# Kernel optimization log

Hardware: AMD Instinct MI355X
Metric: run time of the kernel (lower is better)

## Reference

```python
import jax, jax.numpy as jnp
import numpy as np

B, L, D = 8, 4096, 128
TEMPERATURE = 1.0


def setup_inputs() -> dict:
    key = jax.random.key(0)
    kx, kw, kb = jax.random.split(key, 3)
    x = jax.random.normal(kx, (B, L, D), dtype=jnp.float32)
    # nn.Linear(dim, dim): weight [D, D], bias [D]
    bound = 1.0 / np.sqrt(D)
    W = jax.random.uniform(kw, (D, D), minval=-bound, maxval=bound, dtype=jnp.float32)
    b = jax.random.uniform(kb, (D,), minval=-bound, maxval=bound, dtype=jnp.float32)
    return {"x": x, "W": W, "b": b}


def reference(x, W, b):
    # projected = proj(x): torch Linear is x @ W.T + b
    projected = jnp.einsum("bld,ed->ble", x, W) + b            # [B, L, D]

    # adaptive_avg_pool1d over sequence length L -> L//2 (L even => pair means)
    Bq, Lx, Dx = x.shape
    q = x.reshape(Bq, Lx // 2, 2, Dx).mean(axis=2)             # [B, L/2, D]
    q = jnp.einsum("bld,ed->ble", q, W) + b                    # [B, L/2, D]

    # pairwise squared euclidean distance via ||q||^2 + ||k||^2 - 2 q.k (GEMM form)
    q_sq = jnp.sum(q * q, axis=-1, keepdims=True)              # [B, L/2, 1]
    k_sq = jnp.sum(projected * projected, axis=-1)[:, None, :] # [B, 1, L]
    qk = jnp.einsum("bqd,bkd->bqk", q, projected)              # [B, L/2, L]
    power = jnp.maximum(q_sq + k_sq - 2.0 * qk, 0.0)
    distances = jnp.sqrt(power)
    similarities = jnp.exp(-distances * TEMPERATURE)           # [B, L/2, L]

    k = jnp.einsum("bqk,bkd->bqd", similarities, projected)    # [B, L/2, D]
    v = k
    return (q, k, v)
```

## Files before the change

kernel.cpp:

```cpp
#include <hip/hip_runtime.h>
#include <hip/hip_bf16.h>
#include <stdint.h>

#define NB 8
#define LL 4096
#define LQ 2048
#define DD 128

typedef __attribute__((ext_vector_type(8))) short short8;
typedef __attribute__((ext_vector_type(4))) short short4v;
typedef __attribute__((ext_vector_type(4))) float f4;
typedef __attribute__((ext_vector_type(2))) unsigned int u2;

typedef const __attribute__((address_space(1))) unsigned int guint_t;
typedef __attribute__((address_space(3))) unsigned int luint_t;

__device__ __forceinline__ short8 pack8(const float* v) {
    __hip_bfloat16 h[8];
    #pragma unroll
    for (int j = 0; j < 8; ++j) h[j] = __float2bfloat16(v[j]);
    return *(short8*)h;
}

__global__ __launch_bounds__(256) void projA_kernel(
    const float* __restrict__ x, const float* __restrict__ W,
    const float* __restrict__ bias,
    __hip_bfloat16* __restrict__ proj_sw, __hip_bfloat16* __restrict__ projT,
    __hip_bfloat16* __restrict__ qb, float* __restrict__ qf,
    float* __restrict__ psq, float* __restrict__ qsq)
{
    __shared__ __hip_bfloat16 Wlds[128 * 128];
    __shared__ __hip_bfloat16 Tt[4][128 * 16];

    const int tid = threadIdx.x;
    const int lane = tid & 63, w = tid >> 6;
    const int lr = lane & 15, lh = lane >> 4;

    #pragma unroll
    for (int k = 0; k < 16; ++k) {
        const int f = k * 1024 + tid * 4;
        const int e = f >> 7, col = f & 127;
        f4 v = *(const f4*)&W[f];
        __hip_bfloat16 h[4];
        #pragma unroll
        for (int j = 0; j < 4; ++j) h[j] = __float2bfloat16(v[j]);
        const int byte = e * 256 + (((col * 2)) ^ ((e & 7) << 4));
        *(u2*)((char*)Wlds + byte) = *(u2*)h;
    }
    float bv[8];
    #pragma unroll
    for (int nt = 0; nt < 8; ++nt) bv[nt] = bias[nt * 16 + lr];
    __syncthreads();

    const int tile = blockIdx.x;
    const int row0 = tile * 64 + w * 16;
    const bool qmode = tile >= (NB * LL / 64);

    short8 a[4];
    if (!qmode) {
        const float* src = x + (size_t)(row0 + lr) * DD;
        #pragma unroll
        for (int ks = 0; ks < 4; ++ks) {
            float t[8];
            *(f4*)&t[0] = *(const f4*)&src[ks * 32 + lh * 8];
            *(f4*)&t[4] = *(const f4*)&src[ks * 32 + lh * 8 + 4];
            a[ks] = pack8(t);
        }
    } else {
        const int gq = row0 - NB * LL + lr;
        const int b = gq >> 11, l = gq & 2047;
        const float* s0 = x + ((size_t)b * LL + 2 * l) * DD;
        #pragma unroll
        for (int ks = 0; ks < 4; ++ks) {
            float t[8];
            f4 u0 = *(const f4*)&s0[ks * 32 + lh * 8];
            f4 u1 = *(const f4*)&s0[ks * 32 + lh * 8 + 4];
            f4 v0 = *(const f4*)&s0[DD + ks * 32 + lh * 8];
            f4 v1 = *(const f4*)&s0[DD + ks * 32 + lh * 8 + 4];
            *(f4*)&t[0] = (u0 + v0) * 0.5f;
            *(f4*)&t[4] = (u1 + v1) * 0.5f;
            a[ks] = pack8(t);
        }
    }

    f4 acc[8] = {};
    #pragma unroll
    for (int nt = 0; nt < 8; ++nt) {
        const int e = nt * 16 + lr;
        #pragma unroll
        for (int ks = 0; ks < 4; ++ks) {
            const int byte = e * 256 + ((ks * 64 + lh * 16) ^ ((lr & 7) << 4));
            short8 bk = *(const short8*)((char*)Wlds + byte);
            acc[nt] = __builtin_amdgcn_mfma_f32_16x16x32_bf16(a[ks], bk, acc[nt], 0, 0, 0);
        }
    }

    __hip_bfloat16 h[8][4];
    f4 rn = {0.f, 0.f, 0.f, 0.f};
    #pragma unroll
    for (int nt = 0; nt < 8; ++nt)
        #pragma unroll
        for (int r = 0; r < 4; ++r) {
            float v = acc[nt][r] + bv[nt];
            acc[nt][r] = v;
            h[nt][r] = __float2bfloat16(v);
            float vb = __bfloat162float(h[nt][r]);
            rn[r] += vb * vb;
        }
    #pragma unroll
    for (int m = 1; m < 16; m <<= 1) {
        #pragma unroll
        for (int r = 0; r < 4; ++r) rn[r] += __shfl_xor(rn[r], m);
    }

    if (!qmode) {
        const int gr = row0;
        #pragma unroll
        for (int nt = 0; nt < 8; ++nt)
            #pragma unroll
            for (int r = 0; r < 4; ++r) {
                const int row = gr + lh * 4 + r;
                const int byte = (nt * 32 + lr * 2) ^ (((lh * 4 + r) & 7) << 4);
                *(__hip_bfloat16*)((char*)proj_sw + (size_t)row * 256 + byte) = h[nt][r];
            }
        if (lr == 0) *(f4*)&psq[gr + lh * 4] = rn;
        #pragma unroll
        for (int nt = 0; nt < 8; ++nt) {
            __hip_bfloat16 p[4] = {h[nt][0], h[nt][1], h[nt][2], h[nt][3]};
            *(u2*)((char*)&Tt[w][0] + (nt * 16 + lr) * 32 + lh * 8) = *(u2*)p;
        }
        const int b = gr >> 12, l0 = gr & 4095;
        #pragma unroll
        for (int i = 0; i < 2; ++i) {
            const int e = lane + i * 64;
            short8 t0 = *(const short8*)&Tt[w][e * 16];
            short8 t1 = *(const short8*)&Tt[w][e * 16 + 8];
            __hip_bfloat16* dst = projT + ((size_t)(b * DD + e)) * LL + l0;
            *(short8*)dst = t0;
            *(short8*)(dst + 8) = t1;
        }
    } else {
        const int gq = row0 - NB * LL;
        #pragma unroll
        for (int nt = 0; nt < 8; ++nt)
            #pragma unroll
            for (int r = 0; r < 4; ++r) {
                const size_t idx = (size_t)(gq + lh * 4 + r) * DD + nt * 16 + lr;
                qb[idx] = h[nt][r];
                qf[idx] = acc[nt][r];
            }
        if (lr == 0) *(f4*)&qsq[gq + lh * 4] = rn;
    }
}

__global__ __launch_bounds__(512, 4) void fused_kernel(
    const __hip_bfloat16* __restrict__ proj_sw, const __hip_bfloat16* __restrict__ projT,
    const __hip_bfloat16* __restrict__ qb, const float* __restrict__ psq,
    const float* __restrict__ qsq,
    float* __restrict__ pp0, float* __restrict__ pp1,
    float* __restrict__ pp2, float* __restrict__ pp3, int keys_per)
{
    __shared__ __hip_bfloat16 pbuf[2][4096];
    __shared__ __hip_bfloat16 tbuf[2][128 * 36];
    __shared__ float psbuf[2048];

    const int bid = blockIdx.x;
    const int b = bid & 7;
    const int qt16 = (bid >> 3) & 15;
    const int ks = bid >> 7;
    const int tid = threadIdx.x;
    const int w = tid >> 6, lane = tid & 63;
    const int lr = lane & 15, lh = lane >> 4;

    const int qrow0 = qt16 * 128 + w * 16;
    const int key0 = ks * keys_per;
    const int ntiles = keys_per / 32;

    const char* psw = (const char*)proj_sw + (size_t)b * LL * 256;
    const __hip_bfloat16* ptb = projT + (size_t)b * DD * LL;
    const float* psb = psq + b * LL;

    for (int i = tid; i < keys_per; i += 512) psbuf[i] = psb[key0 + i];

    short8 aq[4];
    const __hip_bfloat16* qbase = qb + ((size_t)b * LQ + qrow0) * DD;
    #pragma unroll
    for (int kss = 0; kss < 4; ++kss)
        aq[kss] = *(const short8*)&qbase[(size_t)lr * DD + kss * 32 + lh * 8];
    const float qn = qsq[b * LQ + qrow0 + lr];

    const int sd = tid >> 2, ss = tid & 3;

    __builtin_amdgcn_global_load_lds(
        (guint_t*)(psw + (size_t)key0 * 256 + w * 1024 + lane * 16),
        (luint_t*)&pbuf[0][w * 512], 16, 0, 0);
    {
        short8 t0 = *(const short8*)(ptb + (size_t)sd * LL + key0 + ss * 8);
        *(short8*)((char*)tbuf[0] + sd * 72 + ss * 16) = t0;
    }
    __syncthreads();

    f4 oc[8] = {};
    int p = 0;

    for (int t = 0; t < ntiles; ++t) {
        short8 tnext;
        if (t + 1 < ntiles) {
            __builtin_amdgcn_global_load_lds(
                (guint_t*)(psw + (size_t)(key0 + (t + 1) * 32) * 256 + w * 1024 + lane * 16),
                (luint_t*)&pbuf[p ^ 1][w * 512], 16, 0, 0);
            tnext = *(const short8*)(ptb + (size_t)sd * LL + key0 + (t + 1) * 32 + ss * 8);
        }

        f4 s[2] = {};
        #pragma unroll
        for (int kss = 0; kss < 4; ++kss) {
            const int off = kss * 64 + lh * 16;
            short8 ak0 = *(const short8*)((char*)pbuf[p] + lr * 256 + (off ^ ((lr & 7) << 4)));
            short8 ak1 = *(const short8*)((char*)pbuf[p] + (16 + lr) * 256 + (off ^ ((lr & 7) << 4)));
            s[0] = __builtin_amdgcn_mfma_f32_16x16x32_bf16(ak0, aq[kss], s[0], 0, 0, 0);
            s[1] = __builtin_amdgcn_mfma_f32_16x16x32_bf16(ak1, aq[kss], s[1], 0, 0, 0);
        }

        f4 pn0 = *(const f4*)&psbuf[t * 32 + lh * 4];
        f4 pn1 = *(const f4*)&psbuf[t * 32 + 16 + lh * 4];
        short8 pa;
        {
            __hip_bfloat16 hh[8];
            #pragma unroll
            for (int r = 0; r < 4; ++r) {
                float p0 = fmaxf(qn + pn0[r] - 2.0f * s[0][r], 1e-20f);
                float p1 = fmaxf(qn + pn1[r] - 2.0f * s[1][r], 1e-20f);
                float d0 = p0 * __frsqrt_rn(p0);
                float d1 = p1 * __frsqrt_rn(p1);
                hh[r]     = __float2bfloat16(__expf(-d0));
                hh[4 + r] = __float2bfloat16(__expf(-d1));
            }
            pa = *(short8*)hh;
        }

        #pragma unroll
        for (int dt = 0; dt < 8; ++dt) {
            const char* rowp = (const char*)tbuf[p] + (dt * 16 + lr) * 72;
            union { short8 v; short4v h[2]; } u;
            u.h[0] = *(const short4v*)(rowp + lh * 8);
            u.h[1] = *(const short4v*)(rowp + 32 + lh * 8);
            oc[dt] = __builtin_amdgcn_mfma_f32_16x16x32_bf16(pa, u.v, oc[dt], 0, 0, 0);
        }

        if (t + 1 < ntiles)
            *(short8*)((char*)tbuf[p ^ 1] + sd * 72 + ss * 16) = tnext;
        __syncthreads();
        p ^= 1;
    }

    float* pb = (ks == 0) ? pp0 : (ks == 1) ? pp1 : (ks == 2) ? pp2 : pp3;
    #pragma unroll
    for (int dt = 0; dt < 8; ++dt)
        #pragma unroll
        for (int r = 0; r < 4; ++r)
            pb[((size_t)b * LQ + qrow0 + lh * 4 + r) * DD + dt * 16 + lr] = oc[dt][r];
}

__global__ __launch_bounds__(256) void reduce_kernel(
    const float* __restrict__ p0, const float* __restrict__ p1,
    const float* __restrict__ p2, const float* __restrict__ p3,
    float* __restrict__ outk, float* __restrict__ outv, int nsplit)
{
    const int b = blockIdx.x & 7;
    const size_t j = (size_t)b * (LQ * DD) + ((size_t)(blockIdx.x >> 3) * 256 + threadIdx.x) * 4;
    f4 v = *(const f4*)&p0[j] + *(const f4*)&p1[j];
    if (nsplit == 4) v += *(const f4*)&p2[j] + *(const f4*)&p3[j];
    *(f4*)&outk[j] = v;
    *(f4*)&outv[j] = v;
}

extern "C" void kernel_launch(void* const* d_in, const int* in_sizes, int n_in,
                              void* d_out, int out_size, void* d_ws, size_t ws_size,
                              hipStream_t stream) {
    const float* x = (const float*)d_in[0];
    const float* W = (const float*)d_in[1];
    const float* bias = (const float*)d_in[2];

    float* out = (float*)d_out;
    const size_t NQ = (size_t)NB * LQ * DD;
    float* qf = out;
    float* outk = out + NQ;
    float* outv = out + 2 * NQ;

    char* ws = (char*)d_ws;
    __hip_bfloat16* proj  = (__hip_bfloat16*)ws;
    __hip_bfloat16* projT = (__hip_bfloat16*)(ws + 8u * 1024 * 1024);
    __hip_bfloat16* qb    = (__hip_bfloat16*)(ws + 16u * 1024 * 1024);
    float* psq            = (float*)(ws + 20u * 1024 * 1024);
    float* qsq            = (float*)(ws + 20u * 1024 * 1024 + 256u * 1024);
    float* pw2            = (float*)(ws + 24u * 1024 * 1024);
    float* pw3            = (float*)(ws + 32u * 1024 * 1024);

    const int nsplit = (ws_size >= (40ull << 20)) ? 4 : 2;
    const int keys_per = LL / nsplit;

    hipLaunchKernelGGL(projA_kernel, dim3((NB * LL + NB * LQ) / 64), dim3(256), 0, stream,
                       x, W, bias, proj, projT, qb, qf, psq, qsq);
    hipLaunchKernelGGL(fused_kernel, dim3(128 * nsplit), dim3(512), 0, stream,
                       proj, projT, qb, psq, qsq, outk, outv, pw2, pw3, keys_per);
    hipLaunchKernelGGL(reduce_kernel, dim3(2048), dim3(256), 0, stream,
                       outk, outv, pw2, pw3, outk, outv, nsplit);
}
```

Measured before the change: 79.89 us.

## Stage projT via async global_load_lds with swizzled layout and 64-key tiles

projA now writes the transposed projection in an XOR-swizzled 64-key-chunk layout. This lets the fused kernel load both operands with global_load_lds directly into LDS instead of going through registers. Key tiles grow from 32 to 64 and the loop uses a two-deep prefetch with manual vmcnt waits and raw barriers. MFMA sections are wrapped in s_setprio. The aim is to cut register-staged loads and barrier overhead and hide global latency, at the cost of twice the LDS per block, which may reduce occupancy.

```diff
diff --git a/kernel.cpp b/kernel.cpp
--- a/kernel.cpp
+++ b/kernel.cpp
@@ -25,7 +25,7 @@
 __global__ __launch_bounds__(256) void projA_kernel(
     const float* __restrict__ x, const float* __restrict__ W,
     const float* __restrict__ bias,
-    __hip_bfloat16* __restrict__ proj_sw, __hip_bfloat16* __restrict__ projT,
+    __hip_bfloat16* __restrict__ proj_sw, __hip_bfloat16* __restrict__ projT_sw,
     __hip_bfloat16* __restrict__ qb, float* __restrict__ qf,
     float* __restrict__ psq, float* __restrict__ qsq)
 {
@@ -133,11 +133,15 @@
         #pragma unroll
         for (int i = 0; i < 2; ++i) {
             const int e = lane + i * 64;
-            short8 t0 = *(const short8*)&Tt[w][e * 16];
-            short8 t1 = *(const short8*)&Tt[w][e * 16 + 8];
-            __hip_bfloat16* dst = projT + ((size_t)(b * DD + e)) * LL + l0;
-            *(short8*)dst = t0;
-            *(short8*)(dst + 8) = t1;
+            const int sw = (e & 15) << 3;
+            char* rowbase = (char*)projT_sw + ((size_t)(b * DD + e)) * (LL * 2)
+                          + (size_t)(l0 & ~63) * 2;
+            const int ob = (l0 & 63) * 2;
+            #pragma unroll
+            for (int c = 0; c < 4; ++c) {
+                u2 chunk = *(u2*)((char*)&Tt[w][e * 16] + c * 8);
+                *(u2*)(rowbase + ((ob + c * 8) ^ sw)) = chunk;
+            }
         }
     } else {
         const int gq = row0 - NB * LL;
@@ -154,15 +158,15 @@
 }
 
 __global__ __launch_bounds__(512, 4) void fused_kernel(
-    const __hip_bfloat16* __restrict__ proj_sw, const __hip_bfloat16* __restrict__ projT,
+    const __hip_bfloat16* __restrict__ proj_sw, const __hip_bfloat16* __restrict__ projT_sw,
     const __hip_bfloat16* __restrict__ qb, const float* __restrict__ psq,
     const float* __restrict__ qsq,
     float* __restrict__ pp0, float* __restrict__ pp1,
     float* __restrict__ pp2, float* __restrict__ pp3, int keys_per)
 {
-    __shared__ __hip_bfloat16 pbuf[2][4096];
-    __shared__ __hip_bfloat16 tbuf[2][128 * 36];
-    __shared__ float psbuf[2048];
+    __shared__ __hip_bfloat16 pbuf[2][8192];
+    __shared__ __hip_bfloat16 tbuf[2][8192];
+    __shared__ __align__(16) float psbuf[2048];
 
     const int bid = blockIdx.x;
     const int b = bid & 7;
@@ -174,10 +178,10 @@
 
     const int qrow0 = qt16 * 128 + w * 16;
     const int key0 = ks * keys_per;
-    const int ntiles = keys_per / 32;
+    const int ntiles = keys_per / 64;
 
     const char* psw = (const char*)proj_sw + (size_t)b * LL * 256;
-    const __hip_bfloat16* ptb = projT + (size_t)b * DD * LL;
+    const char* ptbsw = (const char*)projT_sw + (size_t)b * DD * LL * 2;
     const float* psb = psq + b * LL;
 
     for (int i = tid; i < keys_per; i += 512) psbuf[i] = psb[key0 + i];
@@ -189,68 +193,81 @@
         aq[kss] = *(const short8*)&qbase[(size_t)lr * DD + kss * 32 + lh * 8];
     const float qn = qsq[b * LQ + qrow0 + lr];
 
-    const int sd = tid >> 2, ss = tid & 3;
-
-    __builtin_amdgcn_global_load_lds(
-        (guint_t*)(psw + (size_t)key0 * 256 + w * 1024 + lane * 16),
-        (luint_t*)&pbuf[0][w * 512], 16, 0, 0);
-    {
-        short8 t0 = *(const short8*)(ptb + (size_t)sd * LL + key0 + ss * 8);
-        *(short8*)((char*)tbuf[0] + sd * 72 + ss * 16) = t0;
-    }
     __syncthreads();
+
+    auto stage = [&](int t, int buf) {
+        const size_t kb = (size_t)(key0 + t * 64);
+        #pragma unroll
+        for (int j = 0; j < 2; ++j)
+            __builtin_amdgcn_global_load_lds(
+                (guint_t*)(psw + kb * 256 + (w * 2 + j) * 1024 + lane * 16),
+                (luint_t*)&pbuf[buf][(w * 2 + j) * 512 + lane * 8], 16, 0, 0);
+        #pragma unroll
+        for (int j = 0; j < 2; ++j) {
+            const int row = w * 16 + j * 8 + (lane >> 3);
+            __builtin_amdgcn_global_load_lds(
+                (guint_t*)(ptbsw + (size_t)row * (LL * 2) + kb * 2 + (lane & 7) * 16),
+                (luint_t*)&tbuf[buf][(w * 16 + j * 8) * 64 + lane * 8], 16, 0, 0);
+        }
+    };
+
+    stage(0, 0);
+    stage(1, 1);
 
     f4 oc[8] = {};
     int p = 0;
 
     for (int t = 0; t < ntiles; ++t) {
-        short8 tnext;
-        if (t + 1 < ntiles) {
-            __builtin_amdgcn_global_load_lds(
-                (guint_t*)(psw + (size_t)(key0 + (t + 1) * 32) * 256 + w * 1024 + lane * 16),
-                (luint_t*)&pbuf[p ^ 1][w * 512], 16, 0, 0);
-            tnext = *(const short8*)(ptb + (size_t)sd * LL + key0 + (t + 1) * 32 + ss * 8);
-        }
-
-        f4 s[2] = {};
-        #pragma unroll
-        for (int kss = 0; kss < 4; ++kss) {
-            const int off = kss * 64 + lh * 16;
-            short8 ak0 = *(const short8*)((char*)pbuf[p] + lr * 256 + (off ^ ((lr & 7) << 4)));
-            short8 ak1 = *(const short8*)((char*)pbuf[p] + (16 + lr) * 256 + (off ^ ((lr & 7) << 4)));
-            s[0] = __builtin_amdgcn_mfma_f32_16x16x32_bf16(ak0, aq[kss], s[0], 0, 0, 0);
-            s[1] = __builtin_amdgcn_mfma_f32_16x16x32_bf16(ak1, aq[kss], s[1], 0, 0, 0);
-        }
-
-        f4 pn0 = *(const f4*)&psbuf[t * 32 + lh * 4];
-        f4 pn1 = *(const f4*)&psbuf[t * 32 + 16 + lh * 4];
-        short8 pa;
-        {
-            __hip_bfloat16 hh[8];
-            #pragma unroll
-            for (int r = 0; r < 4; ++r) {
-                float p0 = fmaxf(qn + pn0[r] - 2.0f * s[0][r], 1e-20f);
-                float p1 = fmaxf(qn + pn1[r] - 2.0f * s[1][r], 1e-20f);
-                float d0 = p0 * __frsqrt_rn(p0);
-                float d1 = p1 * __frsqrt_rn(p1);
-                hh[r]     = __float2bfloat16(__expf(-d0));
-                hh[4 + r] = __float2bfloat16(__expf(-d1));
-            }
-            pa = *(short8*)hh;
-        }
-
-        #pragma unroll
-        for (int dt = 0; dt < 8; ++dt) {
-            const char* rowp = (const char*)tbuf[p] + (dt * 16 + lr) * 72;
-            union { short8 v; short4v h[2]; } u;
-            u.h[0] = *(const short4v*)(rowp + lh * 8);
-            u.h[1] = *(const short4v*)(rowp + 32 + lh * 8);
-            oc[dt] = __builtin_amdgcn_mfma_f32_16x16x32_bf16(pa, u.v, oc[dt], 0, 0, 0);
-        }
-
-        if (t + 1 < ntiles)
-            *(short8*)((char*)tbuf[p ^ 1] + sd * 72 + ss * 16) = tnext;
-        __syncthreads();
+        if (t + 1 < ntiles) asm volatile("s_waitcnt vmcnt(4)" ::: "memory");
+        else                asm volatile("s_waitcnt vmcnt(0)" ::: "memory");
+        asm volatile("s_barrier" ::: "memory");
+
+        #pragma unroll
+        for (int sub = 0; sub < 2; ++sub) {
+            f4 s[2] = {};
+            __builtin_amdgcn_s_setprio(1);
+            #pragma unroll
+            for (int kss = 0; kss < 4; ++kss) {
+                const int off = (kss * 64 + lh * 16) ^ ((lr & 7) << 4);
+                short8 ak0 = *(const short8*)((const char*)pbuf[p] + (sub * 32 + lr) * 256 + off);
+                short8 ak1 = *(const short8*)((const char*)pbuf[p] + (sub * 32 + 16 + lr) * 256 + off);
+                s[0] = __builtin_amdgcn_mfma_f32_16x16x32_bf16(ak0, aq[kss], s[0], 0, 0, 0);
+                s[1] = __builtin_amdgcn_mfma_f32_16x16x32_bf16(ak1, aq[kss], s[1], 0, 0, 0);
+            }
+            __builtin_amdgcn_s_setprio(0);
+
+            f4 pn0 = *(const f4*)&psbuf[t * 64 + sub * 32 + lh * 4];
+            f4 pn1 = *(const f4*)&psbuf[t * 64 + sub * 32 + 16 + lh * 4];
+            short8 pa;
+            {
+                __hip_bfloat16 hh[8];
+                #pragma unroll
+                for (int r = 0; r < 4; ++r) {
+                    float p0 = fmaxf(qn + pn0[r] - 2.0f * s[0][r], 1e-20f);
+                    float p1 = fmaxf(qn + pn1[r] - 2.0f * s[1][r], 1e-20f);
+                    float d0 = p0 * __frsqrt_rn(p0);
+                    float d1 = p1 * __frsqrt_rn(p1);
+                    hh[r]     = __float2bfloat16(__expf(-d0));
+                    hh[4 + r] = __float2bfloat16(__expf(-d1));
+                }
+                pa = *(short8*)hh;
+            }
+
+            __builtin_amdgcn_s_setprio(1);
+            #pragma unroll
+            for (int dt = 0; dt < 8; ++dt) {
+                const char* rowp = (const char*)tbuf[p] + (dt * 16 + lr) * 128;
+                const int sw = lr << 3;
+                union { short8 v; short4v h[2]; } u;
+                u.h[0] = *(const short4v*)(rowp + ((lh * 8 + sub * 64) ^ sw));
+                u.h[1] = *(const short4v*)(rowp + ((lh * 8 + 32 + sub * 64) ^ sw));
+                oc[dt] = __builtin_amdgcn_mfma_f32_16x16x32_bf16(pa, u.v, oc[dt], 0, 0, 0);
+            }
+            __builtin_amdgcn_s_setprio(0);
+        }
+
+        asm volatile("s_barrier" ::: "memory");
+        if (t + 2 < ntiles) stage(t + 2, p);
         p ^= 1;
     }
 
```

Measured after the change: 78.75 us. Within noise of the previous version (-1.4%).
